# Kernel optimization log

Hardware: AMD Instinct MI355X
Metric: run time of the kernel (lower is better)

## Reference

```python
import jax, jax.numpy as jnp
import numpy as np

B, SIZE, E = 256, 64, 4096
DEPTH = 2
ADDITIONAL = 16


def _forward(input, keys, offset, sampled_bits):
    b, s, e = input.shape
    m = SIZE >> DEPTH  # section size at this depth
    # choices: first row = round(offset), rest = sampled bits  -> (b, n, s)
    first = jax.lax.stop_gradient(jnp.round(offset)).astype(jnp.int32)[:, None, :]
    choices = jnp.concatenate([first, sampled_bits.astype(jnp.int32)], axis=1)
    n = choices.shape[1]
    # probability of each full choice vector: prod_i (offset_i if c_i else 1-offset_i)
    off = offset[:, None, :]  # (b,1,s)
    p = jnp.where(choices == 1, off, 1.0 - off)  # (b,n,s)
    probs = jnp.prod(p, axis=2, keepdims=True)  # (b,n,1)
    probs = probs / jnp.sum(probs, axis=1, keepdims=True)
    probs = jnp.broadcast_to(probs, (b, n, s))
    # util.split: element at position i (section sec, in-section pos pin) goes to
    # top half (pin//2) or bottom half (m//2 + pin//2) of its section.
    i = jnp.arange(s)
    sec = (i // m) * m
    pin = i % m
    out0 = sec + pin // 2
    out1 = sec + m // 2 + pin // 2
    indices = jnp.where(choices == 1, out1[None, None, :], out0[None, None, :])  # (b,n,s)
    # duplicates: choice rows determine index rows bijectively, so compare choice rows.
    # mark all occurrences except the first (matches stable-sort-based dedup).
    eq = jnp.all(choices[:, :, None, :] == choices[:, None, :, :], axis=-1)  # (b,n,n)
    earlier = jnp.triu(jnp.ones((n, n), dtype=bool), 1)  # mask_{i,j}: i < j
    dups = jnp.any(eq & earlier[None], axis=1)  # (b,n)
    probs = jnp.where(dups[:, :, None], 0.0, probs)
    # batched sparse matmul via dense scatter of the (s,s) matrix per batch
    rows = indices.reshape(b, -1)  # (b, n*s)
    cols = jnp.broadcast_to(i[None, None, :], (b, n, s)).reshape(b, -1)
    vals = probs.reshape(b, -1).astype(input.dtype)
    bidx = jnp.arange(b)[:, None]
    M = jnp.zeros((b, s, s), input.dtype).at[bidx, rows, cols].add(vals)  # (b,s,s)
    output = jnp.einsum('brc,bce->bre', M, input)  # (b,s,e)
    keys_out = jnp.einsum('brc,bc->br', M, keys)   # (b,s)
    return output, keys_out


def setup_inputs() -> dict:
    key = jax.random.key(0)
    k1, k2, k3, k4 = jax.random.split(key, 4)
    return {
        'input': jax.random.normal(k1, (B, SIZE, E), jnp.float32),
        'keys': jax.random.normal(k2, (B, SIZE), jnp.float32),
        'offset': jax.random.uniform(k3, (B, SIZE), jnp.float32),
        'sampled_bits': jax.random.randint(k4, (B, ADDITIONAL, SIZE), 0, 2, jnp.int32),
    }


def reference(input, keys, offset, sampled_bits):
    return _forward(input, keys, offset, sampled_bits)
```

## Files before the change

kernel.cpp:

```cpp
#include <hip/hip_runtime.h>

#define BB     256
#define S      64
#define EE     4096
#define NROWS  17

typedef float f32x4 __attribute__((ext_vector_type(4)));

__global__ __launch_bounds__(64) void split_weights_kernel(
    const float* __restrict__ keys,
    const float* __restrict__ offset,
    const int*   __restrict__ bits,
    float* __restrict__ W0,
    float* __restrict__ W1,
    float* __restrict__ keys_out)
{
    const int b    = blockIdx.x;
    const int lane = threadIdx.x;

    const float off = offset[b * S + lane];
    int bitv[16];
    #pragma unroll
    for (int j = 0; j < 16; ++j)
        bitv[j] = bits[((size_t)b * 16 + j) * S + lane];

    const int loc = lane & 15;
    const int sec = lane & ~15;
    const int t   = loc >> 3;
    const int q   = loc & 7;
    const int c0  = sec + 2 * q;
    const int c1  = c0 + 1;
    const float k0 = keys[b * S + c0];
    const float k1 = keys[b * S + c1];

    unsigned long long mask[NROWS];
    mask[0] = __ballot((int)rintf(off) == 1);
    #pragma unroll
    for (int j = 0; j < 16; ++j)
        mask[1 + j] = __ballot(bitv[j] == 1);

    const float one_m_off = 1.0f - off;
    float prob[NROWS];
    #pragma unroll
    for (int j = 0; j < NROWS; ++j) {
        float v = ((mask[j] >> lane) & 1ull) ? off : one_m_off;
        #pragma unroll
        for (int d = 1; d < 64; d <<= 1)
            v *= __shfl_xor(v, d, 64);
        prob[j] = v;
    }

    float sum = 0.0f;
    #pragma unroll
    for (int j = 0; j < NROWS; ++j) sum += prob[j];
    const float inv = 1.0f / sum;
    #pragma unroll
    for (int j = 0; j < NROWS; ++j) {
        bool dup = false;
        #pragma unroll
        for (int k = 0; k < NROWS; ++k)
            if (k < j) dup |= (mask[k] == mask[j]);
        prob[j] = dup ? 0.0f : prob[j] * inv;
    }

    float w0 = 0.0f, w1 = 0.0f;
    #pragma unroll
    for (int j = 0; j < NROWS; ++j) {
        if ((mask[j] >> lane) & 1ull) w1 += prob[j]; else w0 += prob[j];
    }
    W0[b * S + lane] = w0;
    W1[b * S + lane] = w1;

    const float wa0 = __shfl(w0, c0, 64), wa1 = __shfl(w1, c0, 64);
    const float wb0 = __shfl(w0, c1, 64), wb1 = __shfl(w1, c1, 64);
    const float wa = t ? wa1 : wa0;
    const float wb = t ? wb1 : wb0;
    keys_out[b * S + lane] = wa * k0 + wb * k1;
}

__global__ __launch_bounds__(256) void split_apply_kernel(
    const float* __restrict__ input,
    const float* __restrict__ W0,
    const float* __restrict__ W1,
    float* __restrict__ out)
{
    const int blk = blockIdx.x;
    const int b   = blk >> 5;
    const int pr  = blk & 31;
    const int sec = (pr >> 3) << 4;
    const int q   = pr & 7;
    const int c0  = sec + 2 * q;
    const int c1  = c0 + 1;
    const int r0  = sec + q;
    const int r1  = sec + 8 + q;

    const float wa0 = W0[b * S + c0], wb0 = W0[b * S + c1];
    const float wa1 = W1[b * S + c0], wb1 = W1[b * S + c1];

    const f32x4* __restrict__ in0 = (const f32x4*)(input + ((size_t)b * S + c0) * EE);
    const f32x4* __restrict__ in1 = (const f32x4*)(input + ((size_t)b * S + c1) * EE);
    f32x4* __restrict__ o0 = (f32x4*)(out + ((size_t)b * S + r0) * EE);
    f32x4* __restrict__ o1 = (f32x4*)(out + ((size_t)b * S + r1) * EE);

    const int tid = threadIdx.x;

    f32x4 x0[4], x1[4];
    #pragma unroll
    for (int it = 0; it < 4; ++it) {
        x0[it] = __builtin_nontemporal_load(&in0[tid + it * 256]);
        x1[it] = __builtin_nontemporal_load(&in1[tid + it * 256]);
    }

    #pragma unroll
    for (int it = 0; it < 4; ++it) {
        const int idx = tid + it * 256;
        f32x4 y0, y1;
        y0.x = wa0 * x0[it].x + wb0 * x1[it].x;
        y0.y = wa0 * x0[it].y + wb0 * x1[it].y;
        y0.z = wa0 * x0[it].z + wb0 * x1[it].z;
        y0.w = wa0 * x0[it].w + wb0 * x1[it].w;
        y1.x = wa1 * x0[it].x + wb1 * x1[it].x;
        y1.y = wa1 * x0[it].y + wb1 * x1[it].y;
        y1.z = wa1 * x0[it].z + wb1 * x1[it].z;
        y1.w = wa1 * x0[it].w + wb1 * x1[it].w;
        __builtin_nontemporal_store(y0, &o0[idx]);
        __builtin_nontemporal_store(y1, &o1[idx]);
    }
}

extern "C" void kernel_launch(void* const* d_in, const int* in_sizes, int n_in,
                              void* d_out, int out_size, void* d_ws, size_t ws_size,
                              hipStream_t stream) {
    const float* input  = (const float*)d_in[0];
    const float* keys   = (const float*)d_in[1];
    const float* offset = (const float*)d_in[2];
    const int*   bits   = (const int*)  d_in[3];

    float* out      = (float*)d_out;
    float* keys_out = out + (size_t)BB * S * EE;

    float* W0 = (float*)d_ws;
    float* W1 = W0 + BB * S;

    split_weights_kernel<<<BB, 64, 0, stream>>>(keys, offset, bits, W0, W1, keys_out);
    split_apply_kernel<<<BB * 32, 256, 0, stream>>>(input, W0, W1, out);
}
```

Before: 95.28 us.

## Fuse weight computation into apply kernel, recomputing weights per wave

```diff
diff --git a/kernel.cpp b/kernel.cpp
--- a/kernel.cpp
+++ b/kernel.cpp
@@ -7,16 +7,27 @@
 
 typedef float f32x4 __attribute__((ext_vector_type(4)));
 
-__global__ __launch_bounds__(64) void split_weights_kernel(
+__global__ __launch_bounds__(256) void split_fused_kernel(
+    const float* __restrict__ input,
     const float* __restrict__ keys,
     const float* __restrict__ offset,
     const int*   __restrict__ bits,
-    float* __restrict__ W0,
-    float* __restrict__ W1,
+    float* __restrict__ out,
     float* __restrict__ keys_out)
 {
-    const int b    = blockIdx.x;
-    const int lane = threadIdx.x;
+    const int blk  = blockIdx.x;
+    const int b    = blk >> 5;
+    const int pr   = blk & 31;
+    const int tid  = threadIdx.x;
+    const int lane = tid & 63;
+    const int wv   = tid >> 6;
+
+    const int sec = (pr >> 3) << 4;
+    const int q   = pr & 7;
+    const int c0  = sec + 2 * q;
+    const int c1  = c0 + 1;
+    const int r0  = sec + q;
+    const int r1  = sec + 8 + q;
 
     const float off = offset[b * S + lane];
     int bitv[16];
@@ -24,14 +35,26 @@
     for (int j = 0; j < 16; ++j)
         bitv[j] = bits[((size_t)b * 16 + j) * S + lane];
 
-    const int loc = lane & 15;
-    const int sec = lane & ~15;
-    const int t   = loc >> 3;
-    const int q   = loc & 7;
-    const int c0  = sec + 2 * q;
-    const int c1  = c0 + 1;
-    const float k0 = keys[b * S + c0];
-    const float k1 = keys[b * S + c1];
+    const int kloc = lane & 15;
+    const int ksec = lane & ~15;
+    const int kt   = kloc >> 3;
+    const int kq   = kloc & 7;
+    const int kc0  = ksec + 2 * kq;
+    const int kc1  = kc0 + 1;
+    float k0 = 0.0f, k1 = 0.0f;
+    if (pr == 0 && wv == 0) {
+        k0 = keys[b * S + kc0];
+        k1 = keys[b * S + kc1];
+    }
+
+    const f32x4* __restrict__ in0 = (const f32x4*)(input + ((size_t)b * S + c0) * EE);
+    const f32x4* __restrict__ in1 = (const f32x4*)(input + ((size_t)b * S + c1) * EE);
+    f32x4 x0[4], x1[4];
+    #pragma unroll
+    for (int it = 0; it < 4; ++it) {
+        x0[it] = __builtin_nontemporal_load(&in0[tid + it * 256]);
+        x1[it] = __builtin_nontemporal_load(&in1[tid + it * 256]);
+    }
 
     unsigned long long mask[NROWS];
     mask[0] = __ballot((int)rintf(off) == 1);
@@ -68,48 +91,20 @@
     for (int j = 0; j < NROWS; ++j) {
         if ((mask[j] >> lane) & 1ull) w1 += prob[j]; else w0 += prob[j];
     }
-    W0[b * S + lane] = w0;
-    W1[b * S + lane] = w1;
 
-    const float wa0 = __shfl(w0, c0, 64), wa1 = __shfl(w1, c0, 64);
-    const float wb0 = __shfl(w0, c1, 64), wb1 = __shfl(w1, c1, 64);
-    const float wa = t ? wa1 : wa0;
-    const float wb = t ? wb1 : wb0;
-    keys_out[b * S + lane] = wa * k0 + wb * k1;
-}
+    const float wa0 = __shfl(w0, c0, 64), wb0 = __shfl(w0, c1, 64);
+    const float wa1 = __shfl(w1, c0, 64), wb1 = __shfl(w1, c1, 64);
 
-__global__ __launch_bounds__(256) void split_apply_kernel(
-    const float* __restrict__ input,
-    const float* __restrict__ W0,
-    const float* __restrict__ W1,
-    float* __restrict__ out)
-{
-    const int blk = blockIdx.x;
-    const int b   = blk >> 5;
-    const int pr  = blk & 31;
-    const int sec = (pr >> 3) << 4;
-    const int q   = pr & 7;
-    const int c0  = sec + 2 * q;
-    const int c1  = c0 + 1;
-    const int r0  = sec + q;
-    const int r1  = sec + 8 + q;
+    if (pr == 0 && wv == 0) {
+        const float ka0 = __shfl(w0, kc0, 64), ka1 = __shfl(w1, kc0, 64);
+        const float kb0 = __shfl(w0, kc1, 64), kb1 = __shfl(w1, kc1, 64);
+        const float wa = kt ? ka1 : ka0;
+        const float wb = kt ? kb1 : kb0;
+        keys_out[b * S + lane] = wa * k0 + wb * k1;
+    }
 
-    const float wa0 = W0[b * S + c0], wb0 = W0[b * S + c1];
-    const float wa1 = W1[b * S + c0], wb1 = W1[b * S + c1];
-
-    const f32x4* __restrict__ in0 = (const f32x4*)(input + ((size_t)b * S + c0) * EE);
-    const f32x4* __restrict__ in1 = (const f32x4*)(input + ((size_t)b * S + c1) * EE);
     f32x4* __restrict__ o0 = (f32x4*)(out + ((size_t)b * S + r0) * EE);
     f32x4* __restrict__ o1 = (f32x4*)(out + ((size_t)b * S + r1) * EE);
-
-    const int tid = threadIdx.x;
-
-    f32x4 x0[4], x1[4];
-    #pragma unroll
-    for (int it = 0; it < 4; ++it) {
-        x0[it] = __builtin_nontemporal_load(&in0[tid + it * 256]);
-        x1[it] = __builtin_nontemporal_load(&in1[tid + it * 256]);
-    }
 
     #pragma unroll
     for (int it = 0; it < 4; ++it) {
@@ -139,9 +134,6 @@
     float* out      = (float*)d_out;
     float* keys_out = out + (size_t)BB * S * EE;
 
-    float* W0 = (float*)d_ws;
-    float* W1 = W0 + BB * S;
-
-    split_weights_kernel<<<BB, 64, 0, stream>>>(keys, offset, bits, W0, W1, keys_out);
-    split_apply_kernel<<<BB * 32, 256, 0, stream>>>(input, W0, W1, out);
+    split_fused_kernel<<<BB * 32, 256, 0, stream>>>(input, keys, offset, bits,
+                                                    out, keys_out);
 }
```

Result: no change. 95.88 us (+0.6%).
